# Kernel optimization log

Hardware: AMD Instinct MI355X
Metric: run time of the kernel (lower is better)

## Reference

```python
import jax, jax.numpy as jnp
import numpy as np

SQRT2 = 1.4142135623730951
INV_SQRT_2PI = 0.3989422804014327

def Phi(x):
    # standard normal CDF
    return 0.5 * (1.0 + jax.lax.erf(x / SQRT2))

def phi(x):
    # standard normal pdf
    return INV_SQRT_2PI * jnp.exp(-0.5 * x * x)

def phip(x):
    # derivative of the standard normal pdf
    return -x * phi(x)


def setup_inputs() -> dict:
    key = jax.random.key(0)
    k1, k2, k3 = jax.random.split(key, 3)
    bs, n, c, d = 4, 256, 96, 2
    xin = jax.random.normal(k1, (bs, n, d), dtype=jnp.float32)
    meanin = jax.random.normal(k2, (bs, n, c), dtype=jnp.float32)
    # SPD spatial covariance: A A^T / n + 0.5 I (eigenvalues >> 1e-6)
    A = jax.random.normal(k3, (bs, n, n), dtype=jnp.float32)
    kin = A @ jnp.swapaxes(A, -1, -2) / n + 0.5 * jnp.eye(n, dtype=jnp.float32)
    return {"xin": xin, "meanin": meanin, "kin": kin}


def reference(xin, meanin, kin):
    bs, n, c = meanin.shape
    eye = jnp.eye(n, dtype=kin.dtype)
    kin = kin + eye * 1e-6
    kdiag = jnp.diagonal(kin, axis1=-2, axis2=-1)            # (bs,n)
    stdin = jnp.sqrt(jnp.clip(kdiag[..., None], 1e-8))       # (bs,n,1)
    z = meanin / stdin
    Phis = Phi(z)
    phis = phi(z)
    Eh = meanin * Phis + stdin * phis                        # (bs,n,c)

    # 2x2 matrix K12 per (i,j): [[k_ii, k_ij], [k_ji, k_jj]] -- kept as scalars
    m00 = kdiag[:, :, None]                                  # (bs,n,1) -> broadcast (bs,n,n)
    m11 = kdiag[:, None, :]
    m01 = kin
    m10 = jnp.swapaxes(kin, -1, -2)

    # matrix square root of 2x2 SPD: (M + sqrt(det) I) / sqrt(tr + 2 sqrt(det))
    det = m00 * m11 - m01 * m10
    tr = m00 + m11
    s = jnp.sqrt(jnp.clip(det, 1e-8))
    t = jnp.clip(jnp.sqrt(tr + 2.0 * s), 1e-8)
    s00 = (m00 + s) / t
    s01 = m01 / t
    s10 = m10 / t
    s11 = (m11 + s) / t

    # inverse of the 2x2 sqrt
    dS = jnp.clip(s00 * s11 - s01 * s10, 1e-8)
    i00 = s11 / dS
    i01 = -s01 / dS
    i10 = -s10 / dS
    i11 = s00 / dS

    mi = meanin[:, :, None, :]                               # (bs,n,1,c)
    mj = meanin[:, None, :, :]                               # (bs,1,n,c)

    u1 = i00[..., None] * mi + i01[..., None] * mj           # (bs,n,n,c)
    u2 = i10[..., None] * mi + i11[..., None] * mj
    Phi1 = Phi(u1)
    Phi2 = Phi(u2)
    p1 = phi(u1)
    p2 = phi(u2)

    Psi = Phi1 * Phi2
    psi1 = p1 * Phi2
    psi2 = Phi1 * p2

    EhhT_Psi = (mi * mj + kin[..., None]) * Psi
    EhhT_psi1 = (mj * s00[..., None] + mi * s10[..., None]) * psi1
    EhhT_psi2 = (mj * s01[..., None] + mi * s11[..., None]) * psi2

    SHPhiS11 = s00[..., None] * s01[..., None] * phip(u1) * Phi2
    SHPhiS12 = s01[..., None] * s01[..., None] * p1 * p2
    SHPhiS22 = s01[..., None] * s11[..., None] * Phi1 * phip(u2)
    SHPhiS = SHPhiS11 + 2.0 * SHPhiS12 + SHPhiS22

    EhhT = EhhT_Psi + (EhhT_psi1 + EhhT_psi2) + SHPhiS
    covar = (EhhT - Eh[:, :, None, :] * Eh[:, None, :, :]).mean(-1)   # (bs,n,n)

    dvals = jnp.clip(
        ((meanin ** 2 + stdin ** 2) * Phis + meanin * stdin * phis - Eh ** 2).mean(-1),
        1e-6,
    )                                                        # (bs,n)
    diag_covar = dvals[..., None] * eye                      # diag_embed
    full_covar = jnp.where(diag_covar > 1e-7, diag_covar, covar)
    return (xin, Eh, full_covar + eye * 1e-6)
```

## Files before the change

kernel.cpp:

```cpp
#include <hip/hip_runtime.h>
#include <math.h>

#define BSZ 4
#define NN  256
#define CC  96

#define XIN_OFF  0
#define EH_OFF   2048
#define COV_OFF  100352

#define INV_SQRT_2PI 0.3989422804014327f
#define EXP2C       -0.7213475204444817f
#define PHI_P   0.33267253f
#define PHI_C1  0.1740121f
#define PHI_C2 -0.0479399f
#define PHI_C3  0.3739278f

__device__ __forceinline__ float phi_from_exp_s(float u, float e) {
    float t  = __builtin_amdgcn_rcpf(__builtin_fmaf(PHI_P, fabsf(u), 1.0f));
    float hp = __builtin_fmaf(__builtin_fmaf(PHI_C3, t, PHI_C2), t, PHI_C1) * t * e;
    return 0.5f + __builtin_copysignf(0.5f - hp, u);
}

__global__ __launch_bounds__(128) void relu_cov_row(
    const float* __restrict__ xin, const float* __restrict__ meanin,
    const float* __restrict__ kin, float* __restrict__ out)
{
    const int row = blockIdx.x;
    const int b   = row >> 8;
    const int i   = row & (NN - 1);
    const int tid = threadIdx.x;

    const float kd   = kin[((size_t)b * NN + i) * NN + i] + 1e-6f;
    const float var  = fmaxf(kd, 1e-8f);
    const float stdv = __builtin_amdgcn_sqrtf(var);
    const float rstd = __builtin_amdgcn_rcpf(stdv);

    float dterm = 0.0f;
    if (tid < CC) {
        float m  = meanin[(size_t)row * CC + tid];
        float z  = m * rstd;
        float e  = __builtin_amdgcn_exp2f(z * z * EXP2C);
        float ph = INV_SQRT_2PI * e;
        float Ph = phi_from_exp_s(z, e);
        float Eh = m * Ph + stdv * ph;
        out[EH_OFF + (size_t)row * CC + tid] = Eh;
        dterm = (m * m + var) * Ph + m * stdv * ph - Eh * Eh;
    } else if (tid < CC + 2) {
        int dd = tid - CC;
        out[XIN_OFF + (size_t)row * 2 + dd] = xin[(size_t)row * 2 + dd];
    }

    float v = dterm;
    v += __shfl_down(v, 32, 64);
    v += __shfl_down(v, 16, 64);
    v += __shfl_down(v,  8, 64);
    v += __shfl_down(v,  4, 64);
    v += __shfl_down(v,  2, 64);
    v += __shfl_down(v,  1, 64);
    __shared__ float wsum[2];
    if ((tid & 63) == 0) wsum[tid >> 6] = v;
    __syncthreads();
    if (tid == 0) {
        float dval = fmaxf((wsum[0] + wsum[1]) * (1.0f / 96.0f), 1e-6f);
        out[COV_OFF + ((size_t)b * NN + i) * NN + i] = dval + 1e-6f;
    }
}

__global__ __launch_bounds__(512, 4) void relu_cov_pair(
    const float* __restrict__ meanin, const float* __restrict__ kin,
    const float* __restrict__ Eh, float* __restrict__ out)
{
    const int blk = blockIdx.x;
    const int b   = blk >> 7;
    const int i2  = blk & 127;
    const int tid = threadIdx.x;
    const int p   = tid & 255;
    const int h   = tid >> 8;

    const int rowA = i2;
    const int rowB = 255 - i2;

    __shared__ __align__(16) float smA[CC], sEA[CC], smB[CC], sEB[CC];
    __shared__ float red[512];
    {
        const float* mA = meanin + ((size_t)(b * NN + rowA)) * CC;
        const float* eA = Eh     + ((size_t)(b * NN + rowA)) * CC;
        const float* mB = meanin + ((size_t)(b * NN + rowB)) * CC;
        const float* eB = Eh     + ((size_t)(b * NN + rowB)) * CC;
        if      (tid < 96)  smA[tid]       = mA[tid];
        else if (tid < 192) sEA[tid - 96]  = eA[tid - 96];
        else if (tid < 288) smB[tid - 192] = mB[tid - 192];
        else if (tid < 384) sEB[tid - 288] = eB[tid - 288];
    }
    __syncthreads();

    float acc0 = 0.0f, acc1 = 0.0f;
    if (p < 255) {
        const int  nfirst   = 255 - i2;
        const bool firstSeg = p < nfirst;
        const int  i = firstSeg ? rowA : rowB;
        const int  j = firstSeg ? (i2 + 1 + p) : (p + 1);

        const float* kb  = kin + (size_t)b * NN * NN;
        const float  m00 = kb[i * (NN + 1)] + 1e-6f;
        const float  m11 = kb[j * (NN + 1)] + 1e-6f;
        const float  m01 = kb[i * NN + j];

        const float det = __builtin_fmaf(-m01, m01, m00 * m11);
        const float s   = __builtin_amdgcn_sqrtf(fmaxf(det, 1e-8f));
        const float t   = fmaxf(__builtin_amdgcn_sqrtf(m00 + m11 + 2.0f * s), 1e-8f);
        const float rt  = __builtin_amdgcn_rcpf(t);
        const float s00 = (m00 + s) * rt;
        const float s01 = m01 * rt;
        const float s11 = (m11 + s) * rt;
        const float dS  = fmaxf(__builtin_fmaf(-s01, s01, s00 * s11), 1e-8f);
        const float rdS = __builtin_amdgcn_rcpf(dS);
        const float i00 = s11 * rdS;
        const float i01 = -s01 * rdS;
        const float i11 = s00 * rdS;
        const float qd = -s01 * s01 * s01 * rdS;
        const float qj = s00 * s00 * s11 * rdS;
        const float qi = s00 * s11 * s11 * rdS;
        const float c2 = 2.0f * s01 * s01;

        const float4* mjp = (const float4*)(meanin + ((size_t)(b * NN + j)) * CC + h * 48);
        const float4* Ejp = (const float4*)(Eh     + ((size_t)(b * NN + j)) * CC + h * 48);
        const float4* mip = (const float4*)((firstSeg ? smA : smB) + h * 48);
        const float4* Eip = (const float4*)((firstSeg ? sEA : sEB) + h * 48);

        auto elem = [&](float mi, float mjv, float Ei, float Ej, float& acc) {
            float u1 = __builtin_fmaf(i01, mjv, i00 * mi);
            float u2 = __builtin_fmaf(i11, mjv, i01 * mi);
            float e1 = __builtin_amdgcn_exp2f(u1 * u1 * EXP2C);
            float e2 = __builtin_amdgcn_exp2f(u2 * u2 * EXP2C);
            float d1 = __builtin_fmaf(PHI_P, fabsf(u1), 1.0f);
            float d2 = __builtin_fmaf(PHI_P, fabsf(u2), 1.0f);
            float rp = __builtin_amdgcn_rcpf(d1 * d2);
            float t1 = d2 * rp;
            float t2 = d1 * rp;
            float hp1 = __builtin_fmaf(__builtin_fmaf(PHI_C3, t1, PHI_C2), t1, PHI_C1) * t1 * e1;
            float hp2 = __builtin_fmaf(__builtin_fmaf(PHI_C3, t2, PHI_C2), t2, PHI_C1) * t2 * e2;
            float Phi1 = 0.5f + __builtin_copysignf(0.5f - hp1, u1);
            float Phi2 = 0.5f + __builtin_copysignf(0.5f - hp2, u2);
            float p1 = INV_SQRT_2PI * e1;
            float p2 = INV_SQRT_2PI * e2;
            float a  = __builtin_fmaf(mi, mjv, m01);
            float bb = __builtin_fmaf(qd, mi, qj * mjv);
            float cc = __builtin_fmaf(qi, mi, qd * mjv);
            acc = __builtin_fmaf(a,  Phi1 * Phi2, acc);
            acc = __builtin_fmaf(bb, p1 * Phi2,  acc);
            acc = __builtin_fmaf(cc, Phi1 * p2,  acc);
            acc = __builtin_fmaf(c2, p1 * p2,    acc);
            acc = __builtin_fmaf(-Ei, Ej,        acc);
        };

#pragma unroll 3
        for (int q = 0; q < 12; ++q) {
            float4 mj4 = mjp[q];
            float4 Ej4 = Ejp[q];
            float4 mi4 = mip[q];
            float4 Ei4 = Eip[q];
            elem(mi4.x, mj4.x, Ei4.x, Ej4.x, acc0);
            elem(mi4.y, mj4.y, Ei4.y, Ej4.y, acc1);
            elem(mi4.z, mj4.z, Ei4.z, Ej4.z, acc0);
            elem(mi4.w, mj4.w, Ei4.w, Ej4.w, acc1);
        }
    }

    red[tid] = acc0 + acc1;
    __syncthreads();

    if (tid < 255) {
        float v = (red[tid] + red[tid + 256]) * (1.0f / 96.0f);
        const int nfirst = 255 - i2;
        const int i = (tid < nfirst) ? i2 : (255 - i2);
        const int j = (tid < nfirst) ? (i2 + 1 + tid) : (tid + 1);
        out[COV_OFF + ((size_t)(b * NN + i)) * NN + j] = v;
        out[COV_OFF + ((size_t)(b * NN + j)) * NN + i] = v;
    }
}

extern "C" void kernel_launch(void* const* d_in, const int* in_sizes, int n_in,
                              void* d_out, int out_size, void* d_ws, size_t ws_size,
                              hipStream_t stream) {
    const float* xin    = (const float*)d_in[0];
    const float* meanin = (const float*)d_in[1];
    const float* kin    = (const float*)d_in[2];
    float* out = (float*)d_out;

    relu_cov_row<<<BSZ * NN, 128, 0, stream>>>(xin, meanin, kin, out);
    relu_cov_pair<<<BSZ * 128, 512, 0, stream>>>(meanin, kin, out + EH_OFF, out);
}
```

Baseline: 85.10 us.

## Process full channel range per thread, drop shared-memory reduction in pair kernel

The pair kernel now uses 256 threads per block, with each thread looping over all 96 channels instead of splitting them across two half-blocks. This removes the shared-memory reduction buffer and its second barrier, and eliminates the duplicated per-pair 2x2 sqrt/inverse setup. INV_SQRT_2PI is folded into the per-pair coefficients so the per-element pdf multiplies disappear, and four accumulators break the dependency chain. In exchange the grid has half as many threads in flight, which can reduce latency hiding on a 512-block launch.

```diff
diff --git a/kernel.cpp b/kernel.cpp
--- a/kernel.cpp
+++ b/kernel.cpp
@@ -67,118 +67,106 @@
     }
 }
 
-__global__ __launch_bounds__(512, 4) void relu_cov_pair(
+__global__ __launch_bounds__(256) void relu_cov_pair(
     const float* __restrict__ meanin, const float* __restrict__ kin,
     const float* __restrict__ Eh, float* __restrict__ out)
 {
     const int blk = blockIdx.x;
     const int b   = blk >> 7;
     const int i2  = blk & 127;
-    const int tid = threadIdx.x;
-    const int p   = tid & 255;
-    const int h   = tid >> 8;
+    const int p   = threadIdx.x;
 
     const int rowA = i2;
     const int rowB = 255 - i2;
 
     __shared__ __align__(16) float smA[CC], sEA[CC], smB[CC], sEB[CC];
-    __shared__ float red[512];
     {
         const float* mA = meanin + ((size_t)(b * NN + rowA)) * CC;
         const float* eA = Eh     + ((size_t)(b * NN + rowA)) * CC;
         const float* mB = meanin + ((size_t)(b * NN + rowB)) * CC;
         const float* eB = Eh     + ((size_t)(b * NN + rowB)) * CC;
-        if      (tid < 96)  smA[tid]       = mA[tid];
-        else if (tid < 192) sEA[tid - 96]  = eA[tid - 96];
-        else if (tid < 288) smB[tid - 192] = mB[tid - 192];
-        else if (tid < 384) sEB[tid - 288] = eB[tid - 288];
+        if      (p < 96)  smA[p]       = mA[p];
+        else if (p < 192) sEA[p - 96]  = eA[p - 96];
+        if      (p < 96)  smB[p]       = mB[p];
+        else if (p < 192) sEB[p - 96]  = eB[p - 96];
     }
     __syncthreads();
 
-    float acc0 = 0.0f, acc1 = 0.0f;
-    if (p < 255) {
-        const int  nfirst   = 255 - i2;
-        const bool firstSeg = p < nfirst;
-        const int  i = firstSeg ? rowA : rowB;
-        const int  j = firstSeg ? (i2 + 1 + p) : (p + 1);
+    if (p >= 255) return;
 
-        const float* kb  = kin + (size_t)b * NN * NN;
-        const float  m00 = kb[i * (NN + 1)] + 1e-6f;
-        const float  m11 = kb[j * (NN + 1)] + 1e-6f;
-        const float  m01 = kb[i * NN + j];
+    const int  nfirst   = 255 - i2;
+    const bool firstSeg = p < nfirst;
+    const int  i = firstSeg ? rowA : rowB;
+    const int  j = firstSeg ? (i2 + 1 + p) : (p + 1);
 
-        const float det = __builtin_fmaf(-m01, m01, m00 * m11);
-        const float s   = __builtin_amdgcn_sqrtf(fmaxf(det, 1e-8f));
-        const float t   = fmaxf(__builtin_amdgcn_sqrtf(m00 + m11 + 2.0f * s), 1e-8f);
-        const float rt  = __builtin_amdgcn_rcpf(t);
-        const float s00 = (m00 + s) * rt;
-        const float s01 = m01 * rt;
-        const float s11 = (m11 + s) * rt;
-        const float dS  = fmaxf(__builtin_fmaf(-s01, s01, s00 * s11), 1e-8f);
-        const float rdS = __builtin_amdgcn_rcpf(dS);
-        const float i00 = s11 * rdS;
-        const float i01 = -s01 * rdS;
-        const float i11 = s00 * rdS;
-        const float qd = -s01 * s01 * s01 * rdS;
-        const float qj = s00 * s00 * s11 * rdS;
-        const float qi = s00 * s11 * s11 * rdS;
-        const float c2 = 2.0f * s01 * s01;
+    const float* kb  = kin + (size_t)b * NN * NN;
+    const float  m00 = kb[i * (NN + 1)] + 1e-6f;
+    const float  m11 = kb[j * (NN + 1)] + 1e-6f;
+    const float  m01 = kb[i * NN + j];
 
-        const float4* mjp = (const float4*)(meanin + ((size_t)(b * NN + j)) * CC + h * 48);
-        const float4* Ejp = (const float4*)(Eh     + ((size_t)(b * NN + j)) * CC + h * 48);
-        const float4* mip = (const float4*)((firstSeg ? smA : smB) + h * 48);
-        const float4* Eip = (const float4*)((firstSeg ? sEA : sEB) + h * 48);
+    const float det = __builtin_fmaf(-m01, m01, m00 * m11);
+    const float s   = __builtin_amdgcn_sqrtf(fmaxf(det, 1e-8f));
+    const float t   = fmaxf(__builtin_amdgcn_sqrtf(m00 + m11 + 2.0f * s), 1e-8f);
+    const float rt  = __builtin_amdgcn_rcpf(t);
+    const float s00 = (m00 + s) * rt;
+    const float s01 = m01 * rt;
+    const float s11 = (m11 + s) * rt;
+    const float dS  = fmaxf(__builtin_fmaf(-s01, s01, s00 * s11), 1e-8f);
+    const float rdS = __builtin_amdgcn_rcpf(dS);
+    const float i00 = s11 * rdS;
+    const float i01 = -s01 * rdS;
+    const float i11 = s00 * rdS;
+    const float qd = -INV_SQRT_2PI * s01 * s01 * s01 * rdS;
+    const float qj =  INV_SQRT_2PI * s00 * s00 * s11 * rdS;
+    const float qi =  INV_SQRT_2PI * s00 * s11 * s11 * rdS;
+    const float c2 = 2.0f * INV_SQRT_2PI * INV_SQRT_2PI * s01 * s01;
 
-        auto elem = [&](float mi, float mjv, float Ei, float Ej, float& acc) {
-            float u1 = __builtin_fmaf(i01, mjv, i00 * mi);
-            float u2 = __builtin_fmaf(i11, mjv, i01 * mi);
-            float e1 = __builtin_amdgcn_exp2f(u1 * u1 * EXP2C);
-            float e2 = __builtin_amdgcn_exp2f(u2 * u2 * EXP2C);
-            float d1 = __builtin_fmaf(PHI_P, fabsf(u1), 1.0f);
-            float d2 = __builtin_fmaf(PHI_P, fabsf(u2), 1.0f);
-            float rp = __builtin_amdgcn_rcpf(d1 * d2);
-            float t1 = d2 * rp;
-            float t2 = d1 * rp;
-            float hp1 = __builtin_fmaf(__builtin_fmaf(PHI_C3, t1, PHI_C2), t1, PHI_C1) * t1 * e1;
-            float hp2 = __builtin_fmaf(__builtin_fmaf(PHI_C3, t2, PHI_C2), t2, PHI_C1) * t2 * e2;
-            float Phi1 = 0.5f + __builtin_copysignf(0.5f - hp1, u1);
-            float Phi2 = 0.5f + __builtin_copysignf(0.5f - hp2, u2);
-            float p1 = INV_SQRT_2PI * e1;
-            float p2 = INV_SQRT_2PI * e2;
-            float a  = __builtin_fmaf(mi, mjv, m01);
-            float bb = __builtin_fmaf(qd, mi, qj * mjv);
-            float cc = __builtin_fmaf(qi, mi, qd * mjv);
-            acc = __builtin_fmaf(a,  Phi1 * Phi2, acc);
-            acc = __builtin_fmaf(bb, p1 * Phi2,  acc);
-            acc = __builtin_fmaf(cc, Phi1 * p2,  acc);
-            acc = __builtin_fmaf(c2, p1 * p2,    acc);
-            acc = __builtin_fmaf(-Ei, Ej,        acc);
-        };
+    const float4* mjp = (const float4*)(meanin + ((size_t)(b * NN + j)) * CC);
+    const float4* Ejp = (const float4*)(Eh     + ((size_t)(b * NN + j)) * CC);
+    const float4* mip = (const float4*)(firstSeg ? smA : smB);
+    const float4* Eip = (const float4*)(firstSeg ? sEA : sEB);
 
-#pragma unroll 3
-        for (int q = 0; q < 12; ++q) {
-            float4 mj4 = mjp[q];
-            float4 Ej4 = Ejp[q];
-            float4 mi4 = mip[q];
-            float4 Ei4 = Eip[q];
-            elem(mi4.x, mj4.x, Ei4.x, Ej4.x, acc0);
-            elem(mi4.y, mj4.y, Ei4.y, Ej4.y, acc1);
-            elem(mi4.z, mj4.z, Ei4.z, Ej4.z, acc0);
-            elem(mi4.w, mj4.w, Ei4.w, Ej4.w, acc1);
-        }
+    float acc0 = 0.0f, acc1 = 0.0f, acc2 = 0.0f, acc3 = 0.0f;
+
+    auto elem = [&](float mi, float mjv, float Ei, float Ej, float& acc) {
+        float u1 = __builtin_fmaf(i01, mjv, i00 * mi);
+        float u2 = __builtin_fmaf(i11, mjv, i01 * mi);
+        float e1 = __builtin_amdgcn_exp2f(u1 * u1 * EXP2C);
+        float e2 = __builtin_amdgcn_exp2f(u2 * u2 * EXP2C);
+        float d1 = __builtin_fmaf(PHI_P, fabsf(u1), 1.0f);
+        float d2 = __builtin_fmaf(PHI_P, fabsf(u2), 1.0f);
+        float rp = __builtin_amdgcn_rcpf(d1 * d2);
+        float t1 = d2 * rp;
+        float t2 = d1 * rp;
+        float hp1 = __builtin_fmaf(__builtin_fmaf(PHI_C3, t1, PHI_C2), t1, PHI_C1) * t1 * e1;
+        float hp2 = __builtin_fmaf(__builtin_fmaf(PHI_C3, t2, PHI_C2), t2, PHI_C1) * t2 * e2;
+        float Phi1 = 0.5f + __builtin_copysignf(0.5f - hp1, u1);
+        float Phi2 = 0.5f + __builtin_copysignf(0.5f - hp2, u2);
+        float a  = __builtin_fmaf(mi, mjv, m01);
+        float bb = __builtin_fmaf(qd, mi, qj * mjv);
+        float cc = __builtin_fmaf(qi, mi, qd * mjv);
+        acc = __builtin_fmaf(a,  Phi1 * Phi2, acc);
+        acc = __builtin_fmaf(bb, e1 * Phi2,  acc);
+        acc = __builtin_fmaf(cc, e2 * Phi1,  acc);
+        acc = __builtin_fmaf(c2, e1 * e2,    acc);
+        acc = __builtin_fmaf(-Ei, Ej,        acc);
+    };
+
+#pragma unroll 4
+    for (int q = 0; q < 24; ++q) {
+        float4 mj4 = mjp[q];
+        float4 Ej4 = Ejp[q];
+        float4 mi4 = mip[q];
+        float4 Ei4 = Eip[q];
+        elem(mi4.x, mj4.x, Ei4.x, Ej4.x, acc0);
+        elem(mi4.y, mj4.y, Ei4.y, Ej4.y, acc1);
+        elem(mi4.z, mj4.z, Ei4.z, Ej4.z, acc2);
+        elem(mi4.w, mj4.w, Ei4.w, Ej4.w, acc3);
     }
 
-    red[tid] = acc0 + acc1;
-    __syncthreads();
-
-    if (tid < 255) {
-        float v = (red[tid] + red[tid + 256]) * (1.0f / 96.0f);
-        const int nfirst = 255 - i2;
-        const int i = (tid < nfirst) ? i2 : (255 - i2);
-        const int j = (tid < nfirst) ? (i2 + 1 + tid) : (tid + 1);
-        out[COV_OFF + ((size_t)(b * NN + i)) * NN + j] = v;
-        out[COV_OFF + ((size_t)(b * NN + j)) * NN + i] = v;
-    }
+    float v = ((acc0 + acc1) + (acc2 + acc3)) * (1.0f / 96.0f);
+    out[COV_OFF + ((size_t)(b * NN + i)) * NN + j] = v;
+    out[COV_OFF + ((size_t)(b * NN + j)) * NN + i] = v;
 }
 
 extern "C" void kernel_launch(void* const* d_in, const int* in_sizes, int n_in,
@@ -190,5 +178,5 @@
     float* out = (float*)d_out;
 
     relu_cov_row<<<BSZ * NN, 128, 0, stream>>>(xin, meanin, kin, out);
-    relu_cov_pair<<<BSZ * 128, 512, 0, stream>>>(meanin, kin, out + EH_OFF, out);
+    relu_cov_pair<<<BSZ * 128, 256, 0, stream>>>(meanin, kin, out + EH_OFF, out);
 }
```

New measurement: 87.16 us. +2.4%, slower.
